# Kernel tuning notes

Hardware: AMD Instinct MI355X
Metric: run time of the kernel (lower is better)

Reference implementation:

```python
import jax, jax.numpy as jnp
import numpy as np

B, T, DIM, NH = 2, 2048, 1024, 16
HD = DIM // NH  # 64


def setup_inputs() -> dict:
    key = jax.random.key(0)
    ks = jax.random.split(key, 5)
    x = jax.random.normal(ks[0], (B, T, DIM), dtype=jnp.float32)
    # realistic RoPE tables (any float tables work; use true rotary angles)
    inv_freq = 1.0 / (10000.0 ** (jnp.arange(0, HD, 2, dtype=jnp.float32) / HD))  # [HD/2]
    ang = jnp.arange(T, dtype=jnp.float32)[:, None] * inv_freq[None, :]           # [T, HD/2]
    ang = jnp.repeat(ang, 2, axis=-1)                                             # [T, HD] interleaved pairs
    sin = jnp.sin(ang)[None, None]  # [1,1,T,HD]
    cos = jnp.cos(ang)[None, None]
    W_qkv = jax.random.normal(ks[1], (DIM, 3 * DIM), dtype=jnp.float32) * (DIM ** -0.5)
    W_proj = jax.random.normal(ks[2], (DIM, DIM), dtype=jnp.float32) * (DIM ** -0.5)
    return {"x": x, "sin": sin, "cos": cos, "W_qkv": W_qkv, "W_proj": W_proj}


def _rope(x, sin, cos):
    # x: [B,H,T,D]; sin/cos: [1,1,T,D]
    x1, x2 = x[..., ::2], x[..., 1::2]
    xr = jnp.stack((-x2, x1), axis=-1).reshape(x.shape)  # interleave (-x2, x1)
    return x * cos + xr * sin


def reference(x, sin, cos, W_qkv, W_proj):
    Bx, Tx, C = x.shape
    nh, hd = NH, C // NH
    qkv = x @ W_qkv                                   # [B,T,3C]
    q, k, v = jnp.split(qkv, 3, axis=-1)
    to_bhtd = lambda t: t.reshape(Bx, Tx, nh, hd).transpose(0, 2, 1, 3)
    q, k, v = to_bhtd(q), to_bhtd(k), to_bhtd(v)      # [B,H,T,D]
    q = _rope(q, sin[:, :, :Tx], cos[:, :, :Tx])
    k = _rope(k, sin[:, :, :Tx], cos[:, :, :Tx])
    scale = 1.0 / jnp.sqrt(jnp.asarray(hd, dtype=x.dtype))
    scores = jnp.einsum('bhqd,bhkd->bhqk', q, k) * scale
    causal = jnp.tril(jnp.ones((Tx, Tx), dtype=bool))
    scores = jnp.where(causal, scores, jnp.finfo(scores.dtype).min)
    attn = jax.nn.softmax(scores, axis=-1)
    y = jnp.einsum('bhqk,bhkd->bhqd', attn, v)        # [B,H,T,D]
    y = y.transpose(0, 2, 1, 3).reshape(Bx, Tx, C)
    return y @ W_proj
```

## Files before the change

kernel.cpp:

```cpp
#include <hip/hip_runtime.h>


typedef float  f32x4   __attribute__((ext_vector_type(4)));
typedef float  f32x16  __attribute__((ext_vector_type(16)));
typedef __bf16 bf16x8  __attribute__((ext_vector_type(8)));
typedef short  short8  __attribute__((ext_vector_type(8)));
typedef unsigned uint2v __attribute__((ext_vector_type(2)));
typedef unsigned uint4v __attribute__((ext_vector_type(4)));

#define Bb   2
#define Tt   2048
#define DIMc 1024
#define NHh  16
#define HDd  64

__device__ __forceinline__ short f2bf(float f) {
    unsigned u = __builtin_bit_cast(unsigned, f);
    u += 0x7fffu + ((u >> 16) & 1u);
    return (short)(u >> 16);
}

__device__ __forceinline__ f32x4 mfma16(short8 a, short8 b, f32x4 c) {
    return __builtin_amdgcn_mfma_f32_16x16x32_bf16(
        __builtin_bit_cast(bf16x8, a), __builtin_bit_cast(bf16x8, b), c, 0, 0, 0);
}

__device__ __forceinline__ f32x16 mfma32(short8 a, short8 b, f32x16 c) {
    return __builtin_amdgcn_mfma_f32_32x32x16_bf16(
        __builtin_bit_cast(bf16x8, a), __builtin_bit_cast(bf16x8, b), c, 0, 0, 0);
}

__device__ __forceinline__ unsigned cvtpk(float lo, float hi) {
    unsigned r;
    asm("v_cvt_pk_bf16_f32 %0, %1, %2" : "=v"(r) : "v"(lo), "v"(hi));
    return r;
}

__device__ __forceinline__ void gl_lds16(const void* g, void* l) {
    __builtin_amdgcn_global_load_lds(
        (const __attribute__((address_space(1))) unsigned int*)g,
        (__attribute__((address_space(3))) unsigned int*)l, 16, 0, 0);
}

__global__ __launch_bounds__(256) void convX(const float* __restrict__ X,
                                             short* __restrict__ Xb)
{
    size_t i = ((size_t)blockIdx.x * 256 + threadIdx.x) * 8;
    float4 a = *(const float4*)(X + i);
    float4 b = *(const float4*)(X + i + 4);
    short8 s;
    s[0] = f2bf(a.x); s[1] = f2bf(a.y); s[2] = f2bf(a.z); s[3] = f2bf(a.w);
    s[4] = f2bf(b.x); s[5] = f2bf(b.y); s[6] = f2bf(b.z); s[7] = f2bf(b.w);
    *(short8*)(Xb + i) = s;
}

__global__ __launch_bounds__(256) void convT(const float* __restrict__ W,
                                             short* __restrict__ Wt, int N)
{
    __shared__ float L[64][65];
    const int kb = blockIdx.x * 64, nb = blockIdx.y * 64;
    const int tid = threadIdx.x;
#pragma unroll
    for (int it = 0; it < 4; it++) {
        int kk = it * 16 + (tid >> 4), c = (tid & 15) * 4;
        float4 v = *(const float4*)(W + (size_t)(kb + kk) * N + nb + c);
        L[c + 0][kk] = v.x; L[c + 1][kk] = v.y;
        L[c + 2][kk] = v.z; L[c + 3][kk] = v.w;
    }
    __syncthreads();
#pragma unroll
    for (int it = 0; it < 2; it++) {
        int n = it * 32 + (tid >> 3), ks = (tid & 7) * 8;
        short8 s;
#pragma unroll
        for (int j = 0; j < 8; j++) s[j] = f2bf(L[n][ks + j]);
        *(short8*)(Wt + (size_t)(nb + n) * 1024 + kb + ks) = s;
    }
}

__global__ __launch_bounds__(256, 6) void qkv_rope(
    const short* __restrict__ A, const short* __restrict__ Bt,
    const float* __restrict__ Sn, const float* __restrict__ Cs,
    short* __restrict__ Qo, short* __restrict__ Ko, short* __restrict__ Vt)
{
    __shared__ __align__(16) short LP[64 * 64 + 128 * 64];
    short (*As)[64] = (short(*)[64])LP;
    short (*Bs)[64] = (short(*)[64])(LP + 64 * 64);

    const int bm = blockIdx.x, bn = blockIdx.y;
    const int tid = threadIdx.x;
    const int wv = tid >> 6, lane = tid & 63, g = lane >> 4, l16 = lane & 15;
    const int wr = wv >> 1, wc = wv & 1;
    const int sw = l16 & 7;

    f32x4 acc[2][4];
#pragma unroll
    for (int i = 0; i < 2; i++)
#pragma unroll
        for (int j = 0; j < 4; j++) acc[i][j] = (f32x4){0.f, 0.f, 0.f, 0.f};

    const int sr = tid >> 3, c8 = tid & 7;
    const int gc8 = (c8 ^ (sr & 7)) << 3;
    const short* pA = A  + (size_t)(bm * 64  + sr) * 1024 + gc8;
    const short* pB = Bt + (size_t)(bn * 128 + sr) * 1024 + gc8;

    for (int k0 = 0; k0 < 1024; k0 += 64) {
        gl_lds16(pA + k0,             &As[sr][c8 << 3]);
        gl_lds16(pA + k0 + 32 * 1024, &As[32 + sr][c8 << 3]);
        gl_lds16(pB + k0,             &Bs[sr][c8 << 3]);
        gl_lds16(pB + k0 + 32 * 1024, &Bs[32 + sr][c8 << 3]);
        gl_lds16(pB + k0 + 64 * 1024, &Bs[64 + sr][c8 << 3]);
        gl_lds16(pB + k0 + 96 * 1024, &Bs[96 + sr][c8 << 3]);
        __syncthreads();
#pragma unroll
        for (int ks = 0; ks < 2; ks++) {
            short8 af[2], bfr[4];
#pragma unroll
            for (int mt = 0; mt < 2; mt++)
                af[mt]  = *(const short8*)&As[wr * 32 + mt * 16 + l16][((ks * 4 + g) ^ sw) << 3];
#pragma unroll
            for (int nt = 0; nt < 4; nt++)
                bfr[nt] = *(const short8*)&Bs[wc * 64 + nt * 16 + l16][((ks * 4 + g) ^ sw) << 3];
#pragma unroll
            for (int mt = 0; mt < 2; mt++)
#pragma unroll
                for (int nt = 0; nt < 4; nt++) acc[mt][nt] = mfma16(af[mt], bfr[nt], acc[mt][nt]);
        }
        __syncthreads();
    }

    if (bn >= 16) {
        short (*T)[72] = (short(*)[72])LP;
        const int b  = bm >> 5;
        const int t0 = (bm * 64) & 2047;
        const int nbase = (bn - 16) * 128;
#pragma unroll
        for (int ch = 0; ch < 4; ++ch) {
            __syncthreads();
            if (wc == (ch >> 1)) {
#pragma unroll
                for (int ntl = 0; ntl < 2; ++ntl) {
                    int nt = (ch & 1) * 2 + ntl;
#pragma unroll
                    for (int mt = 0; mt < 2; ++mt)
#pragma unroll
                        for (int r = 0; r < 4; ++r)
                            T[ntl * 16 + l16][wr * 32 + mt * 16 + g * 4 + r] =
                                f2bf(acc[mt][nt][r]);
                }
            }
            __syncthreads();
            int row = tid >> 3, cc8 = (tid & 7) * 8;
            int nn = nbase + ch * 32 + row;
            int h = nn >> 6, d = nn & 63;
            short8 v0 = *(const short8*)&T[row][cc8];
            size_t base = (((size_t)(b * 16 + h) * 64 + d) << 11) + t0 + cc8;
            *(short8*)(Vt + base) = v0;
        }
    } else {
#pragma unroll
        for (int mt = 0; mt < 2; mt++)
#pragma unroll
            for (int nt = 0; nt < 4; nt++)
#pragma unroll
                for (int r = 0; r < 4; r++) {
                    int m = bm * 64 + wr * 32 + mt * 16 + g * 4 + r;
                    int n = bn * 128 + wc * 64 + nt * 16 + l16;
                    float val = acc[mt][nt][r];
                    float partner = __shfl_xor(val, 1, 64);
                    int b = m >> 11, t = m & 2047;
                    int sec = n >> 10, nn = n & 1023;
                    int h = nn >> 6, d = nn & 63;
                    float sv = Sn[t * 64 + d], cv = Cs[t * 64 + d];
                    float ro = (d & 1) ? fmaf(val, cv, partner * sv)
                                       : fmaf(val, cv, -partner * sv);
                    short* dst = (sec == 0) ? Qo : Ko;
                    dst[(((size_t)(b * 16 + h) << 11) + t) * 64 + d] = f2bf(ro);
                }
    }
}

__global__ __launch_bounds__(256, 2) void attn(
    const short* __restrict__ Q, const short* __restrict__ K,
    const short* __restrict__ V, short* __restrict__ Y)
{
    __shared__ __align__(16) short Ks[2][64][64];
    __shared__ __align__(16) short Vs[2][64][64];

    const int bid = blockIdx.x;
    const int xcd = bid & 7, idx = bid >> 3;
    const int bh = xcd * 4 + (idx >> 3);
    const int qb = idx & 7;
    const int tid = threadIdx.x;
    const int wv = tid >> 6, lane = tid & 63;
    const int l5 = lane & 31, hi = lane >> 5;
    const int swl = l5 & 7;

    const short* Qb = Q + (size_t)bh * Tt * 64;
    const short* Kb = K + (size_t)bh * Tt * 64;
    const short* Vb = V + (size_t)bh * 64 * Tt;
    const int b = bh >> 4, h = bh & 15;

    const int srow0 = wv * 16 + (lane >> 3);
    const int sgp   = lane & 7;

    auto stage = [&](int s, int buf) {
        const int k0 = s * 64;
#pragma unroll
        for (int j = 0; j < 2; j++) {
            int row = srow0 + j * 8;
            int gl = sgp ^ (row & 7);
            gl_lds16(Kb + (size_t)(k0 + row) * 64 + gl * 8, &Ks[buf][row][sgp << 3]);
            gl_lds16(Vb + (size_t)row * Tt + k0 + gl * 8,   &Vs[buf][row][sgp << 3]);
        }
    };

    auto run_phase = [&](int qw, int smax_blk) {
        const int q0 = qw * 32, qabs = q0 + l5;
        const int smax_w = qw >> 1;

        short8 qf[4];
#pragma unroll
        for (int c = 0; c < 4; c++)
            qf[c] = *(const short8*)(Qb + (size_t)(q0 + l5) * 64 + c * 16 + hi * 8);

        f32x16 o0, o1;
        float lsum = 0.f;
#pragma unroll
        for (int r = 0; r < 16; r++) { o0[r] = 0.f; o1[r] = 0.f; }

        stage(0, 0);
        __syncthreads();
        for (int s = 0; s <= smax_blk; ++s) {
            if (s < smax_blk) stage(s + 1, (s + 1) & 1);
            if (s <= smax_w) {
                const int buf = s & 1, k0 = s * 64;
                short8 kfa[4], kfb[4];
#pragma unroll
                for (int dg = 0; dg < 4; dg++) {
                    kfa[dg] = *(const short8*)&Ks[buf][l5]     [((((dg << 1) | hi)) ^ swl) << 3];
                    kfb[dg] = *(const short8*)&Ks[buf][32 + l5][((((dg << 1) | hi)) ^ swl) << 3];
                }
                f32x16 sa, sb;
#pragma unroll
                for (int r = 0; r < 16; r++) { sa[r] = 0.f; sb[r] = 0.f; }
#pragma unroll
                for (int dg = 0; dg < 4; dg++) {
                    sa = mfma32(kfa[dg], qf[dg], sa);
                    sb = mfma32(kfb[dg], qf[dg], sb);
                }
                float pA[16], pB[16];
                if (s < smax_w) {
#pragma unroll
                    for (int r = 0; r < 16; r++) {
                        pA[r] = __expf(fmaf(sa[r], 0.125f, -10.f));
                        pB[r] = __expf(fmaf(sb[r], 0.125f, -10.f));
                    }
                } else {
#pragma unroll
                    for (int r = 0; r < 16; r++) {
                        int ka = k0 + (r & 3) + 8 * (r >> 2) + 4 * hi;
                        pA[r] = (ka      <= qabs) ? __expf(fmaf(sa[r], 0.125f, -10.f)) : 0.f;
                        pB[r] = (ka + 32 <= qabs) ? __expf(fmaf(sb[r], 0.125f, -10.f)) : 0.f;
                    }
                }
#pragma unroll
                for (int r = 0; r < 16; r += 4)
                    lsum += ((pA[r] + pA[r + 1]) + (pA[r + 2] + pA[r + 3]))
                          + ((pB[r] + pB[r + 1]) + (pB[r + 2] + pB[r + 3]));

                unsigned wA[8], wB[8];
#pragma unroll
                for (int t = 0; t < 4; t++) {
                    wA[2 * t]     = cvtpk(pA[4 * t],     pA[4 * t + 1]);
                    wA[2 * t + 1] = cvtpk(pA[4 * t + 2], pA[4 * t + 3]);
                    wB[2 * t]     = cvtpk(pB[4 * t],     pB[4 * t + 1]);
                    wB[2 * t + 1] = cvtpk(pB[4 * t + 2], pB[4 * t + 3]);
                }
                uint2v a0 = __builtin_amdgcn_permlane32_swap(wA[0], wA[2], false, false);
                uint2v a1 = __builtin_amdgcn_permlane32_swap(wA[1], wA[3], false, false);
                uint2v a2 = __builtin_amdgcn_permlane32_swap(wA[4], wA[6], false, false);
                uint2v a3 = __builtin_amdgcn_permlane32_swap(wA[5], wA[7], false, false);
                uint2v b0 = __builtin_amdgcn_permlane32_swap(wB[0], wB[2], false, false);
                uint2v b1 = __builtin_amdgcn_permlane32_swap(wB[1], wB[3], false, false);
                uint2v b2 = __builtin_amdgcn_permlane32_swap(wB[4], wB[6], false, false);
                uint2v b3 = __builtin_amdgcn_permlane32_swap(wB[5], wB[7], false, false);
                short8 pav[4];
                { uint4v u = {a0[0], a1[0], a0[1], a1[1]}; pav[0] = __builtin_bit_cast(short8, u); }
                { uint4v u = {a2[0], a3[0], a2[1], a3[1]}; pav[1] = __builtin_bit_cast(short8, u); }
                { uint4v u = {b0[0], b1[0], b0[1], b1[1]}; pav[2] = __builtin_bit_cast(short8, u); }
                { uint4v u = {b2[0], b3[0], b2[1], b3[1]}; pav[3] = __builtin_bit_cast(short8, u); }

#pragma unroll
                for (int ks = 0; ks < 4; ks++) {
                    short8 vf0 = *(const short8*)&Vs[buf][l5]     [((((ks << 1) | hi)) ^ swl) << 3];
                    short8 vf1 = *(const short8*)&Vs[buf][32 + l5][((((ks << 1) | hi)) ^ swl) << 3];
                    o0 = mfma32(pav[ks], vf0, o0);
                    o1 = mfma32(pav[ks], vf1, o1);
                }
            }
            __syncthreads();
        }

        lsum += __shfl_xor(lsum, 32, 64);
        float inv = 1.0f / lsum;
#pragma unroll
        for (int r = 0; r < 16; r++) {
            int ql = (r & 3) + 8 * (r >> 2) + 4 * hi;
            float iv = __shfl(inv, ql, 64);
            size_t row = ((size_t)(b * Tt + q0 + ql)) * DIMc + h * 64;
            Y[row + l5]      = f2bf(o0[r] * iv);
            Y[row + 32 + l5] = f2bf(o1[r] * iv);
        }
    };

    run_phase(qb * 4 + wv, 2 * qb + 1);
    run_phase(63 - qb * 4 - wv, 31 - 2 * qb);
}

__global__ __launch_bounds__(256, 4) void proj(
    const short* __restrict__ A, const short* __restrict__ Bt, float* __restrict__ O)
{
    __shared__ __align__(16) short As[64][64];
    __shared__ __align__(16) short Bs[64][64];
    const int bm = blockIdx.x, bn = blockIdx.y;
    const int tid = threadIdx.x;
    const int wv = tid >> 6, lane = tid & 63, g = lane >> 4, l16 = lane & 15;
    const int wr = wv >> 1, wc = wv & 1;
    const int sw = l16 & 7;

    f32x4 acc[2][2];
#pragma unroll
    for (int i = 0; i < 2; i++)
#pragma unroll
        for (int j = 0; j < 2; j++) acc[i][j] = (f32x4){0.f, 0.f, 0.f, 0.f};

    const int sr = tid >> 3, c8 = tid & 7;
    const int gc8 = (c8 ^ (sr & 7)) << 3;
    const short* pA = A  + (size_t)(bm * 64 + sr) * 1024 + gc8;
    const short* pB = Bt + (size_t)(bn * 64 + sr) * 1024 + gc8;

    for (int k0 = 0; k0 < 1024; k0 += 64) {
        gl_lds16(pA + k0,             &As[sr][c8 << 3]);
        gl_lds16(pA + k0 + 32 * 1024, &As[32 + sr][c8 << 3]);
        gl_lds16(pB + k0,             &Bs[sr][c8 << 3]);
        gl_lds16(pB + k0 + 32 * 1024, &Bs[32 + sr][c8 << 3]);
        __syncthreads();
#pragma unroll
        for (int ks = 0; ks < 2; ks++) {
            short8 af[2], bfr[2];
#pragma unroll
            for (int mt = 0; mt < 2; mt++)
                af[mt]  = *(const short8*)&As[wr * 32 + mt * 16 + l16][((ks * 4 + g) ^ sw) << 3];
#pragma unroll
            for (int nt = 0; nt < 2; nt++)
                bfr[nt] = *(const short8*)&Bs[wc * 32 + nt * 16 + l16][((ks * 4 + g) ^ sw) << 3];
#pragma unroll
            for (int mt = 0; mt < 2; mt++)
#pragma unroll
                for (int nt = 0; nt < 2; nt++) acc[mt][nt] = mfma16(af[mt], bfr[nt], acc[mt][nt]);
        }
        __syncthreads();
    }

#pragma unroll
    for (int mt = 0; mt < 2; mt++)
#pragma unroll
        for (int nt = 0; nt < 2; nt++)
#pragma unroll
            for (int r = 0; r < 4; r++) {
                int m = bm * 64 + wr * 32 + mt * 16 + g * 4 + r;
                int n = bn * 64 + wc * 32 + nt * 16 + l16;
                O[(size_t)m * 1024 + n] = acc[mt][nt][r];
            }
}

extern "C" void kernel_launch(void* const* d_in, const int* in_sizes, int n_in,
                              void* d_out, int out_size, void* d_ws, size_t ws_size,
                              hipStream_t stream)
{
    const float* x     = (const float*)d_in[0];
    const float* sn    = (const float*)d_in[1];
    const float* cs    = (const float*)d_in[2];
    const float* wqkv  = (const float*)d_in[3];
    const float* wproj = (const float*)d_in[4];
    float* out = (float*)d_out;

    char* ws = (char*)d_ws;
    const size_t MB = 1024 * 1024;
    short* q   = (short*)(ws);
    short* k   = (short*)(ws + 8  * MB);
    short* vt  = (short*)(ws + 16 * MB);
    short* y   = (short*)(ws + 24 * MB);
    short* xb  = (short*)(ws + 32 * MB);
    short* wqt = (short*)(ws + 40 * MB);
    short* wpt = (short*)(ws + 46 * MB);

    convX<<<2048, 256, 0, stream>>>(x, xb);
    convT<<<dim3(16, 48), 256, 0, stream>>>(wqkv, wqt, 3072);
    convT<<<dim3(16, 16), 256, 0, stream>>>(wproj, wpt, 1024);
    qkv_rope<<<dim3(64, 24), 256, 0, stream>>>(xb, wqt, sn, cs, q, k, vt);
    attn<<<dim3(256), 256, 0, stream>>>(q, k, vt, y);
    proj<<<dim3(64, 16), 256, 0, stream>>>(y, wpt, out);
}
```

Before: 181.8 us.

## Split attention KV loop across wave pairs and quadruple block count

```diff
diff --git a/kernel.cpp b/kernel.cpp
--- a/kernel.cpp
+++ b/kernel.cpp
@@ -180,7 +180,7 @@
     }
 }
 
-__global__ __launch_bounds__(256, 2) void attn(
+__global__ __launch_bounds__(256, 4) void attn(
     const short* __restrict__ Q, const short* __restrict__ K,
     const short* __restrict__ V, short* __restrict__ Y)
 {
@@ -189,12 +189,17 @@
 
     const int bid = blockIdx.x;
     const int xcd = bid & 7, idx = bid >> 3;
-    const int bh = xcd * 4 + (idx >> 3);
-    const int qb = idx & 7;
+    const int bh = xcd * 4 + (idx >> 5);
+    const int qp = idx & 31;
     const int tid = threadIdx.x;
     const int wv = tid >> 6, lane = tid & 63;
     const int l5 = lane & 31, hi = lane >> 5;
     const int swl = l5 & 7;
+    const int par = wv & 1;
+
+    const int qw = (wv < 2) ? qp : (63 - qp);
+    const int smax_w = qw >> 1;
+    const int smax_blk = 31 - (qp >> 1);
 
     const short* Qb = Q + (size_t)bh * Tt * 64;
     const short* Kb = K + (size_t)bh * Tt * 64;
@@ -215,94 +220,112 @@
         }
     };
 
-    auto run_phase = [&](int qw, int smax_blk) {
-        const int q0 = qw * 32, qabs = q0 + l5;
-        const int smax_w = qw >> 1;
-
-        short8 qf[4];
-#pragma unroll
-        for (int c = 0; c < 4; c++)
-            qf[c] = *(const short8*)(Qb + (size_t)(q0 + l5) * 64 + c * 16 + hi * 8);
-
-        f32x16 o0, o1;
-        float lsum = 0.f;
-#pragma unroll
-        for (int r = 0; r < 16; r++) { o0[r] = 0.f; o1[r] = 0.f; }
-
-        stage(0, 0);
+    const int q0 = qw * 32, qabs = q0 + l5;
+
+    short8 qf[4];
+#pragma unroll
+    for (int c = 0; c < 4; c++)
+        qf[c] = *(const short8*)(Qb + (size_t)(q0 + l5) * 64 + c * 16 + hi * 8);
+
+    f32x16 o0, o1;
+    float lsum = 0.f;
+#pragma unroll
+    for (int r = 0; r < 16; r++) { o0[r] = 0.f; o1[r] = 0.f; }
+
+    stage(0, 0);
+    __syncthreads();
+    for (int s = 0; s <= smax_blk; ++s) {
+        if (s < smax_blk) stage(s + 1, (s + 1) & 1);
+        if ((s & 1) == par && s <= smax_w) {
+            const int buf = s & 1, k0 = s * 64;
+            short8 kfa[4], kfb[4];
+#pragma unroll
+            for (int dg = 0; dg < 4; dg++) {
+                kfa[dg] = *(const short8*)&Ks[buf][l5]     [((((dg << 1) | hi)) ^ swl) << 3];
+                kfb[dg] = *(const short8*)&Ks[buf][32 + l5][((((dg << 1) | hi)) ^ swl) << 3];
+            }
+            f32x16 sa, sb;
+#pragma unroll
+            for (int r = 0; r < 16; r++) { sa[r] = 0.f; sb[r] = 0.f; }
+#pragma unroll
+            for (int dg = 0; dg < 4; dg++) {
+                sa = mfma32(kfa[dg], qf[dg], sa);
+                sb = mfma32(kfb[dg], qf[dg], sb);
+            }
+            float pA[16], pB[16];
+            if (s < smax_w) {
+#pragma unroll
+                for (int r = 0; r < 16; r++) {
+                    pA[r] = __expf(fmaf(sa[r], 0.125f, -10.f));
+                    pB[r] = __expf(fmaf(sb[r], 0.125f, -10.f));
+                }
+            } else {
+#pragma unroll
+                for (int r = 0; r < 16; r++) {
+                    int ka = k0 + (r & 3) + 8 * (r >> 2) + 4 * hi;
+                    pA[r] = (ka      <= qabs) ? __expf(fmaf(sa[r], 0.125f, -10.f)) : 0.f;
+                    pB[r] = (ka + 32 <= qabs) ? __expf(fmaf(sb[r], 0.125f, -10.f)) : 0.f;
+                }
+            }
+#pragma unroll
+            for (int r = 0; r < 16; r += 4)
+                lsum += ((pA[r] + pA[r + 1]) + (pA[r + 2] + pA[r + 3]))
+                      + ((pB[r] + pB[r + 1]) + (pB[r + 2] + pB[r + 3]));
+
+            unsigned wA[8], wB[8];
+#pragma unroll
+            for (int t = 0; t < 4; t++) {
+                wA[2 * t]     = cvtpk(pA[4 * t],     pA[4 * t + 1]);
+                wA[2 * t + 1] = cvtpk(pA[4 * t + 2], pA[4 * t + 3]);
+                wB[2 * t]     = cvtpk(pB[4 * t],     pB[4 * t + 1]);
+                wB[2 * t + 1] = cvtpk(pB[4 * t + 2], pB[4 * t + 3]);
+            }
+            uint2v a0 = __builtin_amdgcn_permlane32_swap(wA[0], wA[2], false, false);
+            uint2v a1 = __builtin_amdgcn_permlane32_swap(wA[1], wA[3], false, false);
+            uint2v a2 = __builtin_amdgcn_permlane32_swap(wA[4], wA[6], false, false);
+            uint2v a3 = __builtin_amdgcn_permlane32_swap(wA[5], wA[7], false, false);
+            uint2v b0 = __builtin_amdgcn_permlane32_swap(wB[0], wB[2], false, false);
+            uint2v b1 = __builtin_amdgcn_permlane32_swap(wB[1], wB[3], false, false);
+            uint2v b2 = __builtin_amdgcn_permlane32_swap(wB[4], wB[6], false, false);
+            uint2v b3 = __builtin_amdgcn_permlane32_swap(wB[5], wB[7], false, false);
+            short8 pav[4];
+            { uint4v u = {a0[0], a1[0], a0[1], a1[1]}; pav[0] = __builtin_bit_cast(short8, u); }
+            { uint4v u = {a2[0], a3[0], a2[1], a3[1]}; pav[1] = __builtin_bit_cast(short8, u); }
+            { uint4v u = {b0[0], b1[0], b0[1], b1[1]}; pav[2] = __builtin_bit_cast(short8, u); }
+            { uint4v u = {b2[0], b3[0], b2[1], b3[1]}; pav[3] = __builtin_bit_cast(short8, u); }
+
+#pragma unroll
+            for (int ks = 0; ks < 4; ks++) {
+                short8 vf0 = *(const short8*)&Vs[buf][l5]     [((((ks << 1) | hi)) ^ swl) << 3];
+                short8 vf1 = *(const short8*)&Vs[buf][32 + l5][((((ks << 1) | hi)) ^ swl) << 3];
+                o0 = mfma32(pav[ks], vf0, o0);
+                o1 = mfma32(pav[ks], vf1, o1);
+            }
+        }
         __syncthreads();
-        for (int s = 0; s <= smax_blk; ++s) {
-            if (s < smax_blk) stage(s + 1, (s + 1) & 1);
-            if (s <= smax_w) {
-                const int buf = s & 1, k0 = s * 64;
-                short8 kfa[4], kfb[4];
-#pragma unroll
-                for (int dg = 0; dg < 4; dg++) {
-                    kfa[dg] = *(const short8*)&Ks[buf][l5]     [((((dg << 1) | hi)) ^ swl) << 3];
-                    kfb[dg] = *(const short8*)&Ks[buf][32 + l5][((((dg << 1) | hi)) ^ swl) << 3];
-                }
-                f32x16 sa, sb;
-#pragma unroll
-                for (int r = 0; r < 16; r++) { sa[r] = 0.f; sb[r] = 0.f; }
-#pragma unroll
-                for (int dg = 0; dg < 4; dg++) {
-                    sa = mfma32(kfa[dg], qf[dg], sa);
-                    sb = mfma32(kfb[dg], qf[dg], sb);
-                }
-                float pA[16], pB[16];
-                if (s < smax_w) {
-#pragma unroll
-                    for (int r = 0; r < 16; r++) {
-                        pA[r] = __expf(fmaf(sa[r], 0.125f, -10.f));
-                        pB[r] = __expf(fmaf(sb[r], 0.125f, -10.f));
-                    }
-                } else {
-#pragma unroll
-                    for (int r = 0; r < 16; r++) {
-                        int ka = k0 + (r & 3) + 8 * (r >> 2) + 4 * hi;
-                        pA[r] = (ka      <= qabs) ? __expf(fmaf(sa[r], 0.125f, -10.f)) : 0.f;
-                        pB[r] = (ka + 32 <= qabs) ? __expf(fmaf(sb[r], 0.125f, -10.f)) : 0.f;
-                    }
-                }
-#pragma unroll
-                for (int r = 0; r < 16; r += 4)
-                    lsum += ((pA[r] + pA[r + 1]) + (pA[r + 2] + pA[r + 3]))
-                          + ((pB[r] + pB[r + 1]) + (pB[r + 2] + pB[r + 3]));
-
-                unsigned wA[8], wB[8];
-#pragma unroll
-                for (int t = 0; t < 4; t++) {
-                    wA[2 * t]     = cvtpk(pA[4 * t],     pA[4 * t + 1]);
-                    wA[2 * t + 1] = cvtpk(pA[4 * t + 2], pA[4 * t + 3]);
-                    wB[2 * t]     = cvtpk(pB[4 * t],     pB[4 * t + 1]);
-                    wB[2 * t + 1] = cvtpk(pB[4 * t + 2], pB[4 * t + 3]);
-                }
-                uint2v a0 = __builtin_amdgcn_permlane32_swap(wA[0], wA[2], false, false);
-                uint2v a1 = __builtin_amdgcn_permlane32_swap(wA[1], wA[3], false, false);
-                uint2v a2 = __builtin_amdgcn_permlane32_swap(wA[4], wA[6], false, false);
-                uint2v a3 = __builtin_amdgcn_permlane32_swap(wA[5], wA[7], false, false);
-                uint2v b0 = __builtin_amdgcn_permlane32_swap(wB[0], wB[2], false, false);
-                uint2v b1 = __builtin_amdgcn_permlane32_swap(wB[1], wB[3], false, false);
-                uint2v b2 = __builtin_amdgcn_permlane32_swap(wB[4], wB[6], false, false);
-                uint2v b3 = __builtin_amdgcn_permlane32_swap(wB[5], wB[7], false, false);
-                short8 pav[4];
-                { uint4v u = {a0[0], a1[0], a0[1], a1[1]}; pav[0] = __builtin_bit_cast(short8, u); }
-                { uint4v u = {a2[0], a3[0], a2[1], a3[1]}; pav[1] = __builtin_bit_cast(short8, u); }
-                { uint4v u = {b0[0], b1[0], b0[1], b1[1]}; pav[2] = __builtin_bit_cast(short8, u); }
-                { uint4v u = {b2[0], b3[0], b2[1], b3[1]}; pav[3] = __builtin_bit_cast(short8, u); }
-
-#pragma unroll
-                for (int ks = 0; ks < 4; ks++) {
-                    short8 vf0 = *(const short8*)&Vs[buf][l5]     [((((ks << 1) | hi)) ^ swl) << 3];
-                    short8 vf1 = *(const short8*)&Vs[buf][32 + l5][((((ks << 1) | hi)) ^ swl) << 3];
-                    o0 = mfma32(pav[ks], vf0, o0);
-                    o1 = mfma32(pav[ks], vf1, o1);
-                }
-            }
-            __syncthreads();
-        }
-
-        lsum += __shfl_xor(lsum, 32, 64);
+    }
+
+    lsum += __shfl_xor(lsum, 32, 64);
+    float* RED = (float*)&Ks[0][0][0];
+    float* RL  = (float*)&Vs[0][0][0];
+    if (par == 1) {
+        int base = (wv >> 1) * 2048;
+#pragma unroll
+        for (int r = 0; r < 16; r++) {
+            RED[base + r * 64 + lane]        = o0[r];
+            RED[base + 1024 + r * 64 + lane] = o1[r];
+        }
+        RL[(wv >> 1) * 64 + lane] = lsum;
+    }
+    __syncthreads();
+    if (par == 0) {
+        int base = (wv >> 1) * 2048;
+#pragma unroll
+        for (int r = 0; r < 16; r++) {
+            o0[r] += RED[base + r * 64 + lane];
+            o1[r] += RED[base + 1024 + r * 64 + lane];
+        }
+        lsum += RL[(wv >> 1) * 64 + lane];
         float inv = 1.0f / lsum;
 #pragma unroll
         for (int r = 0; r < 16; r++) {
@@ -312,10 +335,7 @@
             Y[row + l5]      = f2bf(o0[r] * iv);
             Y[row + 32 + l5] = f2bf(o1[r] * iv);
         }
-    };
-
-    run_phase(qb * 4 + wv, 2 * qb + 1);
-    run_phase(63 - qb * 4 - wv, 31 - 2 * qb);
+    }
 }
 
 __global__ __launch_bounds__(256, 4) void proj(
@@ -400,6 +420,6 @@
     convT<<<dim3(16, 48), 256, 0, stream>>>(wqkv, wqt, 3072);
     convT<<<dim3(16, 16), 256, 0, stream>>>(wproj, wpt, 1024);
     qkv_rope<<<dim3(64, 24), 256, 0, stream>>>(xb, wqt, sn, cs, q, k, vt);
-    attn<<<dim3(256), 256, 0, stream>>>(q, k, vt, y);
+    attn<<<dim3(1024), 256, 0, stream>>>(q, k, vt, y);
     proj<<<dim3(64, 16), 256, 0, stream>>>(y, wpt, out);
 }
```

New measurement: 197.0 us. +8.4%, slower.
